# Optimization experiments

Measured on AMD Instinct MI355X. Metric: run time of the kernel, lower is better.

Reference implementation:

```python
import jax, jax.numpy as jnp
import numpy as np

DROPOUT_P = 0.5


def spmm(edge_weight, src, dst, x, n_nodes):
    # out[i] = sum_{e: dst[e]==i} edge_weight[e] * x[src[e]]  == spmm(adj, x)
    msgs = x[src] * edge_weight[:, None]          # [E, F]
    return jax.ops.segment_sum(msgs, dst, num_segments=n_nodes)


def setup_inputs() -> dict:
    key = jax.random.key(0)
    ks = jax.random.split(key, 7)
    N, E, F_IN, F_HID, F_OUT = 100000, 1600000, 128, 128, 64
    return {
        "x": jax.random.normal(ks[0], (N, F_IN), dtype=jnp.float32),
        "edge_weight": jax.random.uniform(ks[1], (E,), dtype=jnp.float32),
        "W1": jax.random.normal(ks[2], (F_IN, F_HID), dtype=jnp.float32) * 0.05,
        "b1": jnp.zeros((F_HID,), dtype=jnp.float32),
        "W2": jax.random.normal(ks[3], (F_HID, F_OUT), dtype=jnp.float32) * 0.05,
        "b2": jnp.zeros((F_OUT,), dtype=jnp.float32),
        "src": jax.random.randint(ks[4], (E,), 0, N, dtype=jnp.int32),
        "dst": jax.random.randint(ks[5], (E,), 0, N, dtype=jnp.int32),
        "n_nodes": N,
    }


def reference(x, edge_weight, W1, b1, W2, b2, src, dst, n_nodes):
    # layer 1: relu(Linear(spmm(adj, x)))
    h = spmm(edge_weight, src, dst, x, n_nodes)
    h = jax.nn.relu(h @ W1 + b1)
    # dropout (training=True), deterministic fixed key for reproducibility
    keep = jax.random.bernoulli(jax.random.key(42), 1.0 - DROPOUT_P, h.shape)
    h = jnp.where(keep, h / (1.0 - DROPOUT_P), 0.0)
    # layer 2: Linear(spmm(adj, h))
    h = spmm(edge_weight, src, dst, h, n_nodes)
    return h @ W2 + b2
```

## Files before the change

kernel.cpp:

```cpp
#include <hip/hip_runtime.h>

typedef unsigned int u32;
typedef unsigned short u16;
typedef __attribute__((ext_vector_type(8))) short short8;
typedef __attribute__((ext_vector_type(8))) unsigned short u16x8;
typedef __attribute__((ext_vector_type(4))) float f32x4;
typedef __attribute__((ext_vector_type(4))) unsigned short u16x4;

#define CAP 10240

__device__ __forceinline__ u16 f2bf(float f) {
  u32 u = __builtin_bit_cast(u32, f);
  u32 r = (u + 0x7fffu + ((u >> 16) & 1u)) >> 16;
  return (u16)r;
}
__device__ __forceinline__ float bf2f(u32 lo16) {
  return __builtin_bit_cast(float, lo16 << 16);
}

__device__ __forceinline__ void threefry2x32(u32 k0, u32 k1, u32 x0, u32 x1,
                                             u32& y0, u32& y1) {
  const u32 ks2 = k0 ^ k1 ^ 0x1BD11BDAu;
#define TFR(r) { x0 += x1; x1 = (x1 << (r)) | (x1 >> (32 - (r))); x1 ^= x0; }
  x0 += k0; x1 += k1;
  TFR(13) TFR(15) TFR(26) TFR(6)
  x0 += k1; x1 += ks2 + 1u;
  TFR(17) TFR(29) TFR(16) TFR(24)
  x0 += ks2; x1 += k0 + 2u;
  TFR(13) TFR(15) TFR(26) TFR(6)
  x0 += k0; x1 += k1 + 3u;
  TFR(17) TFR(29) TFR(16) TFR(24)
  x0 += k1; x1 += ks2 + 4u;
  TFR(13) TFR(15) TFR(26) TFR(6)
  x0 += ks2; x1 += k0 + 5u;
#undef TFR
  y0 = x0; y1 = x1;
}

__device__ __forceinline__ bool dropout_keep(u32 j) {
  u32 y0, y1;
  threefry2x32(0u, 42u, 0u, j, y0, y1);
  return ((y0 ^ y1) & 0x80000000u) == 0u;
}

__global__ __launch_bounds__(256) void init_bcur(int* __restrict__ bcur) {
  bcur[threadIdx.x] = threadIdx.x * CAP;
}

#define EPB 8192

__global__ __launch_bounds__(256) void stage_edges(
    const int* __restrict__ src, const int* __restrict__ dst,
    const float* __restrict__ ew, int* __restrict__ bcur,
    int2* __restrict__ staged, int E) {
  __shared__ int h[256];
  __shared__ int cb[256];
  int t = threadIdx.x;
  h[t] = 0;
  __syncthreads();
  int base = blockIdx.x * EPB;
  int end = min(base + EPB, E);
  for (int i = base + t; i < end; i += 256)
    atomicAdd(&h[(u32)dst[i] >> 9], 1);
  __syncthreads();
  if (h[t]) cb[t] = atomicAdd(&bcur[t], h[t]);
  h[t] = 0;
  __syncthreads();
  for (int i = base + t; i < end; i += 256) {
    int d = dst[i];
    int b = (u32)d >> 9;
    int loc = atomicAdd(&h[b], 1);
    int pos = cb[b] + loc;
    if (pos < (b + 1) * CAP)
      staged[pos] = make_int2(src[i] | ((d & 511) << 23),
                              __builtin_bit_cast(int, ew[i]));
  }
}

__global__ __launch_bounds__(256) void bucket_sort(
    const int2* __restrict__ staged, const int* __restrict__ bcur,
    int2* __restrict__ rowinfo, int2* __restrict__ epk, int N) {
  __shared__ int cnt[512];
  __shared__ int cur[512];
  __shared__ int sc[256];
  const int t = threadIdx.x;
  const int b = blockIdx.x;
  const int node0 = b << 9;
  const int nn = min(512, N - node0);
  const int ebase = b * CAP;
  const int ecnt = min(bcur[b] - ebase, CAP);
  cnt[t] = 0; cnt[t + 256] = 0;
  __syncthreads();
  for (int i = t; i < ecnt; i += 256)
    atomicAdd(&cnt[(u32)staged[ebase + i].x >> 23], 1);
  __syncthreads();
  int a = cnt[2 * t], c = cnt[2 * t + 1];
  int pa = (a + 1) & ~1, pc = (c + 1) & ~1;
  int s = pa + pc;
  sc[t] = s;
  __syncthreads();
  for (int off = 1; off < 256; off <<= 1) {
    int tmp = (t >= off) ? sc[t - off] : 0;
    __syncthreads();
    sc[t] += tmp;
    __syncthreads();
  }
  int excl = sc[t] - s;
  cur[2 * t] = ebase + excl;
  cur[2 * t + 1] = ebase + excl + pa;
  if (2 * t < nn) rowinfo[node0 + 2 * t] = make_int2(ebase + excl, a);
  if (2 * t + 1 < nn) rowinfo[node0 + 2 * t + 1] = make_int2(ebase + excl + pa, c);
  __syncthreads();
  for (int i = t; i < ecnt; i += 256) {
    int2 p = staged[ebase + i];
    int dl = (u32)p.x >> 23;
    int pos = atomicAdd(&cur[dl], 1);
    epk[pos] = make_int2(p.x & 0x7fffff, p.y);
  }
}

__global__ __launch_bounds__(256) void spmm_csr_f128_bf16(
    const u16* __restrict__ V, const int2* __restrict__ epk,
    const int2* __restrict__ rowinfo, u16* __restrict__ out, int N) {
  int node = blockIdx.x * 8 + (threadIdx.x >> 5);
  if (node >= N) return;
  int l32 = threadIdx.x & 31;
  int2 ri = rowinfo[node];
  int e = ri.x, end = ri.x + ri.y;
  float a0 = 0.f, a1 = 0.f, a2 = 0.f, a3 = 0.f;
  for (; e + 8 <= end; e += 8) {
    int4 pp[4];
#pragma unroll
    for (int k = 0; k < 4; ++k)
      pp[k] = reinterpret_cast<const int4*>(epk + e)[k];
    uint2 v[8];
#pragma unroll
    for (int k = 0; k < 4; ++k) {
      v[2 * k] = reinterpret_cast<const uint2*>(V + (size_t)pp[k].x * 128)[l32];
      v[2 * k + 1] = reinterpret_cast<const uint2*>(V + (size_t)pp[k].z * 128)[l32];
    }
#pragma unroll
    for (int k = 0; k < 4; ++k) {
      float w0 = __builtin_bit_cast(float, pp[k].y);
      float w1 = __builtin_bit_cast(float, pp[k].w);
      a0 = fmaf(bf2f(v[2 * k].x & 0xffffu), w0, a0);
      a1 = fmaf(bf2f(v[2 * k].x >> 16), w0, a1);
      a2 = fmaf(bf2f(v[2 * k].y & 0xffffu), w0, a2);
      a3 = fmaf(bf2f(v[2 * k].y >> 16), w0, a3);
      a0 = fmaf(bf2f(v[2 * k + 1].x & 0xffffu), w1, a0);
      a1 = fmaf(bf2f(v[2 * k + 1].x >> 16), w1, a1);
      a2 = fmaf(bf2f(v[2 * k + 1].y & 0xffffu), w1, a2);
      a3 = fmaf(bf2f(v[2 * k + 1].y >> 16), w1, a3);
    }
  }
  if (e + 4 <= end) {
    int4 pp[2];
#pragma unroll
    for (int k = 0; k < 2; ++k)
      pp[k] = reinterpret_cast<const int4*>(epk + e)[k];
    uint2 v[4];
#pragma unroll
    for (int k = 0; k < 2; ++k) {
      v[2 * k] = reinterpret_cast<const uint2*>(V + (size_t)pp[k].x * 128)[l32];
      v[2 * k + 1] = reinterpret_cast<const uint2*>(V + (size_t)pp[k].z * 128)[l32];
    }
#pragma unroll
    for (int k = 0; k < 2; ++k) {
      float w0 = __builtin_bit_cast(float, pp[k].y);
      float w1 = __builtin_bit_cast(float, pp[k].w);
      a0 = fmaf(bf2f(v[2 * k].x & 0xffffu), w0, a0);
      a1 = fmaf(bf2f(v[2 * k].x >> 16), w0, a1);
      a2 = fmaf(bf2f(v[2 * k].y & 0xffffu), w0, a2);
      a3 = fmaf(bf2f(v[2 * k].y >> 16), w0, a3);
      a0 = fmaf(bf2f(v[2 * k + 1].x & 0xffffu), w1, a0);
      a1 = fmaf(bf2f(v[2 * k + 1].x >> 16), w1, a1);
      a2 = fmaf(bf2f(v[2 * k + 1].y & 0xffffu), w1, a2);
      a3 = fmaf(bf2f(v[2 * k + 1].y >> 16), w1, a3);
    }
    e += 4;
  }
  for (; e < end; ++e) {
    int2 p = epk[e];
    uint2 v = reinterpret_cast<const uint2*>(V + (size_t)p.x * 128)[l32];
    float w = __builtin_bit_cast(float, p.y);
    a0 = fmaf(bf2f(v.x & 0xffffu), w, a0);
    a1 = fmaf(bf2f(v.x >> 16), w, a1);
    a2 = fmaf(bf2f(v.y & 0xffffu), w, a2);
    a3 = fmaf(bf2f(v.y >> 16), w, a3);
  }
  uint2 o;
  o.x = (u32)f2bf(a0) | ((u32)f2bf(a1) << 16);
  o.y = (u32)f2bf(a2) | ((u32)f2bf(a3) << 16);
  reinterpret_cast<uint2*>(out + (size_t)node * 128)[l32] = o;
}

__global__ __launch_bounds__(256) void spmm_csr_f64_bias(
    const u16* __restrict__ V, const int2* __restrict__ epk,
    const int2* __restrict__ rowinfo, const float* __restrict__ b2,
    float* __restrict__ out, int N) {
  int node = blockIdx.x * 16 + (threadIdx.x >> 4);
  if (node >= N) return;
  int l16 = threadIdx.x & 15;
  int2 ri = rowinfo[node];
  int e = ri.x, end = ri.x + ri.y;
  float4 bb = reinterpret_cast<const float4*>(b2)[l16];
  float a0 = bb.x, a1 = bb.y, a2 = bb.z, a3 = bb.w;
  for (; e + 8 <= end; e += 8) {
    int4 pp[4];
#pragma unroll
    for (int k = 0; k < 4; ++k)
      pp[k] = reinterpret_cast<const int4*>(epk + e)[k];
    uint2 v[8];
#pragma unroll
    for (int k = 0; k < 4; ++k) {
      v[2 * k] = reinterpret_cast<const uint2*>(V + (size_t)pp[k].x * 64)[l16];
      v[2 * k + 1] = reinterpret_cast<const uint2*>(V + (size_t)pp[k].z * 64)[l16];
    }
#pragma unroll
    for (int k = 0; k < 4; ++k) {
      float w0 = __builtin_bit_cast(float, pp[k].y);
      float w1 = __builtin_bit_cast(float, pp[k].w);
      a0 = fmaf(bf2f(v[2 * k].x & 0xffffu), w0, a0);
      a1 = fmaf(bf2f(v[2 * k].x >> 16), w0, a1);
      a2 = fmaf(bf2f(v[2 * k].y & 0xffffu), w0, a2);
      a3 = fmaf(bf2f(v[2 * k].y >> 16), w0, a3);
      a0 = fmaf(bf2f(v[2 * k + 1].x & 0xffffu), w1, a0);
      a1 = fmaf(bf2f(v[2 * k + 1].x >> 16), w1, a1);
      a2 = fmaf(bf2f(v[2 * k + 1].y & 0xffffu), w1, a2);
      a3 = fmaf(bf2f(v[2 * k + 1].y >> 16), w1, a3);
    }
  }
  for (; e < end; ++e) {
    int2 p = epk[e];
    uint2 v = reinterpret_cast<const uint2*>(V + (size_t)p.x * 64)[l16];
    float w = __builtin_bit_cast(float, p.y);
    a0 = fmaf(bf2f(v.x & 0xffffu), w, a0);
    a1 = fmaf(bf2f(v.x >> 16), w, a1);
    a2 = fmaf(bf2f(v.y & 0xffffu), w, a2);
    a3 = fmaf(bf2f(v.y >> 16), w, a3);
  }
  reinterpret_cast<float4*>(out + (size_t)node * 64)[l16] =
      make_float4(a0, a1, a2, a3);
}

__global__ __launch_bounds__(256) void gemm_xw1_mfma(
    const float* __restrict__ X, const float* __restrict__ W,
    u16* __restrict__ Y, int N) {
  __shared__ short As[128 * 128];
  __shared__ short Bs[128 * 128];
  const int t = threadIdx.x;
  const int row0 = blockIdx.x << 7;

  for (int i = t; i < 128 * 32; i += 256) {
    int m = i >> 5, k4 = i & 31;
    int r = row0 + m;
    float4 v = make_float4(0.f, 0.f, 0.f, 0.f);
    if (r < N) v = reinterpret_cast<const float4*>(X)[(size_t)r * 32 + k4];
    u16x4 b;
    b.x = f2bf(v.x); b.y = f2bf(v.y); b.z = f2bf(v.z); b.w = f2bf(v.w);
    int off = (m * 128 + (k4 << 2)) ^ ((m & 7) << 3);
    *reinterpret_cast<u16x4*>(&As[off]) = b;
  }
  for (int i = t; i < 128 * 32; i += 256) {
    int k = i >> 5, n4 = i & 31;
    float4 v = reinterpret_cast<const float4*>(W)[(size_t)k * 32 + n4];
    int c0 = n4 << 2;
    Bs[(((c0 + 0) * 128 + k)) ^ (((c0 + 0) & 7) << 3)] = (short)f2bf(v.x);
    Bs[(((c0 + 1) * 128 + k)) ^ (((c0 + 1) & 7) << 3)] = (short)f2bf(v.y);
    Bs[(((c0 + 2) * 128 + k)) ^ (((c0 + 2) & 7) << 3)] = (short)f2bf(v.z);
    Bs[(((c0 + 3) * 128 + k)) ^ (((c0 + 3) & 7) << 3)] = (short)f2bf(v.w);
  }
  __syncthreads();

  const int wid = t >> 6, lane = t & 63;
  const int wr = (wid >> 1) * 64, wc = (wid & 1) * 64;
  const int l15 = lane & 15, lk = (lane >> 4) * 8;

  f32x4 acc[4][4];
#pragma unroll
  for (int m = 0; m < 4; ++m)
#pragma unroll
    for (int n = 0; n < 4; ++n) acc[m][n] = (f32x4)(0.f);

#pragma unroll
  for (int kk = 0; kk < 4; ++kk) {
    const int kb = kk * 32 + lk;
    short8 a[4], b[4];
#pragma unroll
    for (int m = 0; m < 4; ++m) {
      int row = wr + m * 16 + l15;
      a[m] = *reinterpret_cast<const short8*>(&As[(row * 128 + kb) ^ ((row & 7) << 3)]);
    }
#pragma unroll
    for (int n = 0; n < 4; ++n) {
      int col = wc + n * 16 + l15;
      b[n] = *reinterpret_cast<const short8*>(&Bs[(col * 128 + kb) ^ ((col & 7) << 3)]);
    }
#pragma unroll
    for (int m = 0; m < 4; ++m)
#pragma unroll
      for (int n = 0; n < 4; ++n)
        acc[m][n] = __builtin_amdgcn_mfma_f32_16x16x32_bf16(a[m], b[n], acc[m][n], 0, 0, 0);
  }

#pragma unroll
  for (int m = 0; m < 4; ++m) {
    int rbase = row0 + wr + m * 16 + (lane >> 4) * 4;
#pragma unroll
    for (int n = 0; n < 4; ++n) {
      int col = wc + n * 16 + l15;
#pragma unroll
      for (int r = 0; r < 4; ++r) {
        int row = rbase + r;
        if (row < N) Y[(size_t)row * 128 + col] = f2bf(acc[m][n][r]);
      }
    }
  }
}

__global__ __launch_bounds__(256) void gemm_h_w2_mfma(
    const u16* __restrict__ H, const float* __restrict__ bias1,
    const float* __restrict__ W2, u16* __restrict__ O, int N) {
  __shared__ short As[128 * 128];
  __shared__ short Bs[64 * 128];
  const int t = threadIdx.x;
  const int row0 = blockIdx.x << 7;

  for (int i = t; i < 128 * 16; i += 256) {
    int k = i >> 4, n4 = i & 15;
    float4 v = reinterpret_cast<const float4*>(W2)[(size_t)k * 16 + n4];
    int c0 = n4 << 2;
    Bs[(((c0 + 0) * 128 + k)) ^ (((c0 + 0) & 7) << 3)] = (short)f2bf(v.x);
    Bs[(((c0 + 1) * 128 + k)) ^ (((c0 + 1) & 7) << 3)] = (short)f2bf(v.y);
    Bs[(((c0 + 2) * 128 + k)) ^ (((c0 + 2) & 7) << 3)] = (short)f2bf(v.z);
    Bs[(((c0 + 3) * 128 + k)) ^ (((c0 + 3) & 7) << 3)] = (short)f2bf(v.w);
  }

  for (int i = t; i < 128 * 16; i += 256) {
    int m = i >> 4, g = i & 15;
    int r = row0 + m;
    int c0 = g << 3;
    u16x8 o = (u16x8)(0);
    if (r < N) {
      u16x8 v = *reinterpret_cast<const u16x8*>(H + (size_t)r * 128 + c0);
      float4 b0 = reinterpret_cast<const float4*>(bias1)[g * 2];
      float4 b1v = reinterpret_cast<const float4*>(bias1)[g * 2 + 1];
      float bb[8] = {b0.x, b0.y, b0.z, b0.w, b1v.x, b1v.y, b1v.z, b1v.w};
      u32 base = (u32)r * 128u + (u32)c0;
#pragma unroll
      for (int e = 0; e < 8; ++e) {
        float z = fmaxf(bf2f((u16)v[e]) + bb[e], 0.f);
        o[e] = dropout_keep(base + e) ? f2bf(z + z) : (u16)0;
      }
    }
    *reinterpret_cast<u16x8*>(&As[(m * 128 + c0) ^ ((m & 7) << 3)]) = o;
  }
  __syncthreads();

  const int wid = t >> 6, lane = t & 63;
  const int wr = wid * 32;
  const int l15 = lane & 15, lk = (lane >> 4) * 8;

  f32x4 acc[2][4];
#pragma unroll
  for (int m = 0; m < 2; ++m)
#pragma unroll
    for (int n = 0; n < 4; ++n) acc[m][n] = (f32x4)(0.f);

#pragma unroll
  for (int kk = 0; kk < 4; ++kk) {
    const int kb = kk * 32 + lk;
    short8 a[2], b[4];
#pragma unroll
    for (int m = 0; m < 2; ++m) {
      int row = wr + m * 16 + l15;
      a[m] = *reinterpret_cast<const short8*>(&As[(row * 128 + kb) ^ ((row & 7) << 3)]);
    }
#pragma unroll
    for (int n = 0; n < 4; ++n) {
      int col = n * 16 + l15;
      b[n] = *reinterpret_cast<const short8*>(&Bs[(col * 128 + kb) ^ ((col & 7) << 3)]);
    }
#pragma unroll
    for (int m = 0; m < 2; ++m)
#pragma unroll
      for (int n = 0; n < 4; ++n)
        acc[m][n] = __builtin_amdgcn_mfma_f32_16x16x32_bf16(a[m], b[n], acc[m][n], 0, 0, 0);
  }

#pragma unroll
  for (int m = 0; m < 2; ++m) {
    int rbase = row0 + wr + m * 16 + (lane >> 4) * 4;
#pragma unroll
    for (int n = 0; n < 4; ++n) {
      int col = n * 16 + l15;
#pragma unroll
      for (int r = 0; r < 4; ++r) {
        int row = rbase + r;
        if (row < N) O[(size_t)row * 64 + col] = f2bf(acc[m][n][r]);
      }
    }
  }
}

extern "C" void kernel_launch(void* const* d_in, const int* in_sizes, int n_in,
                              void* d_out, int out_size, void* d_ws, size_t ws_size,
                              hipStream_t stream) {
  const float* x  = (const float*)d_in[0];
  const float* ew = (const float*)d_in[1];
  const float* W1 = (const float*)d_in[2];
  const float* b1 = (const float*)d_in[3];
  const float* W2 = (const float*)d_in[4];
  const float* b2 = (const float*)d_in[5];
  const int*   src = (const int*)d_in[6];
  const int*   dst = (const int*)d_in[7];
  const int N = in_sizes[0] / 128;
  const int E = in_sizes[1];
  float* out = (float*)d_out;

  const int nb = (N + 511) >> 9;

  u16*   h1      = (u16*)d_ws;
  u16*   y       = h1 + (size_t)N * 128;
  u16*   h3      = y;
  int2*  staged  = (int2*)(y + (size_t)N * 128);
  int2*  epk     = staged + (size_t)nb * CAP;
  int2*  rowinfo = epk + (size_t)nb * CAP;
  int*   bcur    = (int*)(rowinfo + N + 4);

  const int cBlocks = (E + EPB - 1) / EPB;
  const int gBlocks = (N + 127) / 128;

  init_bcur<<<1, 256, 0, stream>>>(bcur);
  stage_edges<<<cBlocks, 256, 0, stream>>>(src, dst, ew, bcur, staged, E);
  bucket_sort<<<nb, 256, 0, stream>>>(staged, bcur, rowinfo, epk, N);

  gemm_xw1_mfma<<<gBlocks, 256, 0, stream>>>(x, W1, y, N);
  spmm_csr_f128_bf16<<<(N + 7) / 8, 256, 0, stream>>>(y, epk, rowinfo, h1, N);
  gemm_h_w2_mfma<<<gBlocks, 256, 0, stream>>>(h1, b1, W2, h3, N);
  spmm_csr_f64_bias<<<(N + 15) / 16, 256, 0, stream>>>(h3, epk, rowinfo, b2, out, N);
}
```

Measured before the change: 245.9 us.

## Fuse edge staging into X·W1 GEMM launch and shrink buckets to 256 nodes

After: 234.8 us. 1.05x faster.

```diff
diff --git a/kernel.cpp b/kernel.cpp
--- a/kernel.cpp
+++ b/kernel.cpp
@@ -7,7 +7,8 @@
 typedef __attribute__((ext_vector_type(4))) float f32x4;
 typedef __attribute__((ext_vector_type(4))) unsigned short u16x4;
 
-#define CAP 10240
+#define CAP 4864
+#define EPB 8192
 
 __device__ __forceinline__ u16 f2bf(float f) {
   u32 u = __builtin_bit_cast(u32, f);
@@ -43,61 +44,132 @@
   return ((y0 ^ y1) & 0x80000000u) == 0u;
 }
 
-__global__ __launch_bounds__(256) void init_bcur(int* __restrict__ bcur) {
-  bcur[threadIdx.x] = threadIdx.x * CAP;
-}
-
-#define EPB 8192
-
-__global__ __launch_bounds__(256) void stage_edges(
+__global__ __launch_bounds__(256) void gemmA_stage_fused(
+    const float* __restrict__ X, const float* __restrict__ W,
+    u16* __restrict__ Y, int N, int cBlocks,
     const int* __restrict__ src, const int* __restrict__ dst,
     const float* __restrict__ ew, int* __restrict__ bcur,
-    int2* __restrict__ staged, int E) {
-  __shared__ int h[256];
-  __shared__ int cb[256];
-  int t = threadIdx.x;
-  h[t] = 0;
-  __syncthreads();
-  int base = blockIdx.x * EPB;
-  int end = min(base + EPB, E);
-  for (int i = base + t; i < end; i += 256)
-    atomicAdd(&h[(u32)dst[i] >> 9], 1);
-  __syncthreads();
-  if (h[t]) cb[t] = atomicAdd(&bcur[t], h[t]);
-  h[t] = 0;
-  __syncthreads();
-  for (int i = base + t; i < end; i += 256) {
-    int d = dst[i];
-    int b = (u32)d >> 9;
-    int loc = atomicAdd(&h[b], 1);
-    int pos = cb[b] + loc;
-    if (pos < (b + 1) * CAP)
-      staged[pos] = make_int2(src[i] | ((d & 511) << 23),
-                              __builtin_bit_cast(int, ew[i]));
+    int2* __restrict__ staged, int E, int nb) {
+  __shared__ short As[128 * 128];
+  __shared__ short Bs[128 * 128];
+  const int t = threadIdx.x;
+
+  if (blockIdx.x < cBlocks) {
+    int* h  = (int*)As;
+    int* cb = ((int*)As) + 512;
+    for (int j = t; j < nb; j += 256) h[j] = 0;
+    __syncthreads();
+    const int base = blockIdx.x * EPB;
+    const int end = min(base + EPB, E);
+    for (int i = base + t; i < end; i += 256)
+      atomicAdd(&h[(u32)dst[i] >> 8], 1);
+    __syncthreads();
+    for (int j = t; j < nb; j += 256) {
+      cb[j] = h[j] ? atomicAdd(&bcur[j], h[j]) : 0;
+      h[j] = 0;
+    }
+    __syncthreads();
+    for (int i = base + t; i < end; i += 256) {
+      int d = dst[i];
+      int b = (u32)d >> 8;
+      int loc = atomicAdd(&h[b], 1);
+      int pos = cb[b] + loc;
+      if (pos < CAP)
+        staged[(size_t)b * CAP + pos] =
+            make_int2(src[i] | ((d & 255) << 23), __builtin_bit_cast(int, ew[i]));
+    }
+    return;
+  }
+
+  const int row0 = (blockIdx.x - cBlocks) << 7;
+
+  for (int i = t; i < 128 * 32; i += 256) {
+    int m = i >> 5, k4 = i & 31;
+    int r = row0 + m;
+    float4 v = make_float4(0.f, 0.f, 0.f, 0.f);
+    if (r < N) v = reinterpret_cast<const float4*>(X)[(size_t)r * 32 + k4];
+    u16x4 b;
+    b.x = f2bf(v.x); b.y = f2bf(v.y); b.z = f2bf(v.z); b.w = f2bf(v.w);
+    int off = (m * 128 + (k4 << 2)) ^ ((m & 7) << 3);
+    *reinterpret_cast<u16x4*>(&As[off]) = b;
+  }
+  for (int i = t; i < 128 * 32; i += 256) {
+    int k = i >> 5, n4 = i & 31;
+    float4 v = reinterpret_cast<const float4*>(W)[(size_t)k * 32 + n4];
+    int c0 = n4 << 2;
+    Bs[(((c0 + 0) * 128 + k)) ^ (((c0 + 0) & 7) << 3)] = (short)f2bf(v.x);
+    Bs[(((c0 + 1) * 128 + k)) ^ (((c0 + 1) & 7) << 3)] = (short)f2bf(v.y);
+    Bs[(((c0 + 2) * 128 + k)) ^ (((c0 + 2) & 7) << 3)] = (short)f2bf(v.z);
+    Bs[(((c0 + 3) * 128 + k)) ^ (((c0 + 3) & 7) << 3)] = (short)f2bf(v.w);
+  }
+  __syncthreads();
+
+  const int wid = t >> 6, lane = t & 63;
+  const int wr = (wid >> 1) * 64, wc = (wid & 1) * 64;
+  const int l15 = lane & 15, lk = (lane >> 4) * 8;
+
+  f32x4 acc[4][4];
+#pragma unroll
+  for (int m = 0; m < 4; ++m)
+#pragma unroll
+    for (int n = 0; n < 4; ++n) acc[m][n] = (f32x4)(0.f);
+
+#pragma unroll
+  for (int kk = 0; kk < 4; ++kk) {
+    const int kb = kk * 32 + lk;
+    short8 a[4], b[4];
+#pragma unroll
+    for (int m = 0; m < 4; ++m) {
+      int row = wr + m * 16 + l15;
+      a[m] = *reinterpret_cast<const short8*>(&As[(row * 128 + kb) ^ ((row & 7) << 3)]);
+    }
+#pragma unroll
+    for (int n = 0; n < 4; ++n) {
+      int col = wc + n * 16 + l15;
+      b[n] = *reinterpret_cast<const short8*>(&Bs[(col * 128 + kb) ^ ((col & 7) << 3)]);
+    }
+#pragma unroll
+    for (int m = 0; m < 4; ++m)
+#pragma unroll
+      for (int n = 0; n < 4; ++n)
+        acc[m][n] = __builtin_amdgcn_mfma_f32_16x16x32_bf16(a[m], b[n], acc[m][n], 0, 0, 0);
+  }
+
+#pragma unroll
+  for (int m = 0; m < 4; ++m) {
+    int rbase = row0 + wr + m * 16 + (lane >> 4) * 4;
+#pragma unroll
+    for (int n = 0; n < 4; ++n) {
+      int col = wc + n * 16 + l15;
+#pragma unroll
+      for (int r = 0; r < 4; ++r) {
+        int row = rbase + r;
+        if (row < N) Y[(size_t)row * 128 + col] = f2bf(acc[m][n][r]);
+      }
+    }
   }
 }
 
 __global__ __launch_bounds__(256) void bucket_sort(
     const int2* __restrict__ staged, const int* __restrict__ bcur,
     int2* __restrict__ rowinfo, int2* __restrict__ epk, int N) {
-  __shared__ int cnt[512];
-  __shared__ int cur[512];
+  __shared__ int cnt[256];
+  __shared__ int cur[256];
   __shared__ int sc[256];
   const int t = threadIdx.x;
   const int b = blockIdx.x;
-  const int node0 = b << 9;
-  const int nn = min(512, N - node0);
+  const int node0 = b << 8;
+  const int nn = min(256, N - node0);
   const int ebase = b * CAP;
-  const int ecnt = min(bcur[b] - ebase, CAP);
-  cnt[t] = 0; cnt[t + 256] = 0;
+  const int ecnt = min(bcur[b], CAP);
+  cnt[t] = 0;
   __syncthreads();
   for (int i = t; i < ecnt; i += 256)
     atomicAdd(&cnt[(u32)staged[ebase + i].x >> 23], 1);
   __syncthreads();
-  int a = cnt[2 * t], c = cnt[2 * t + 1];
-  int pa = (a + 1) & ~1, pc = (c + 1) & ~1;
-  int s = pa + pc;
-  sc[t] = s;
+  int a = cnt[t];
+  int pa = (a + 1) & ~1;
+  sc[t] = pa;
   __syncthreads();
   for (int off = 1; off < 256; off <<= 1) {
     int tmp = (t >= off) ? sc[t - off] : 0;
@@ -105,11 +177,9 @@
     sc[t] += tmp;
     __syncthreads();
   }
-  int excl = sc[t] - s;
-  cur[2 * t] = ebase + excl;
-  cur[2 * t + 1] = ebase + excl + pa;
-  if (2 * t < nn) rowinfo[node0 + 2 * t] = make_int2(ebase + excl, a);
-  if (2 * t + 1 < nn) rowinfo[node0 + 2 * t + 1] = make_int2(ebase + excl + pa, c);
+  int excl = sc[t] - pa;
+  cur[t] = ebase + excl;
+  if (t < nn) rowinfo[node0 + t] = make_int2(ebase + excl, a);
   __syncthreads();
   for (int i = t; i < ecnt; i += 256) {
     int2 p = staged[ebase + i];
@@ -118,6 +188,18 @@
     epk[pos] = make_int2(p.x & 0x7fffff, p.y);
   }
 }
+
+#define F128_FMA2(VA, VB, W0, W1)                      \
+  { float w0 = __builtin_bit_cast(float, W0);          \
+    float w1 = __builtin_bit_cast(float, W1);          \
+    a0 = fmaf(bf2f((VA).x & 0xffffu), w0, a0);         \
+    a1 = fmaf(bf2f((VA).x >> 16), w0, a1);             \
+    a2 = fmaf(bf2f((VA).y & 0xffffu), w0, a2);         \
+    a3 = fmaf(bf2f((VA).y >> 16), w0, a3);             \
+    a0 = fmaf(bf2f((VB).x & 0xffffu), w1, a0);         \
+    a1 = fmaf(bf2f((VB).x >> 16), w1, a1);             \
+    a2 = fmaf(bf2f((VB).y & 0xffffu), w1, a2);         \
+    a3 = fmaf(bf2f((VB).y >> 16), w1, a3); }
 
 __global__ __launch_bounds__(256) void spmm_csr_f128_bf16(
     const u16* __restrict__ V, const int2* __restrict__ epk,
@@ -128,32 +210,22 @@
   int2 ri = rowinfo[node];
   int e = ri.x, end = ri.x + ri.y;
   float a0 = 0.f, a1 = 0.f, a2 = 0.f, a3 = 0.f;
-  for (; e + 8 <= end; e += 8) {
-    int4 pp[4];
-#pragma unroll
-    for (int k = 0; k < 4; ++k)
+  for (; e + 16 <= end; e += 16) {
+    int4 pp[8];
+#pragma unroll
+    for (int k = 0; k < 8; ++k)
       pp[k] = reinterpret_cast<const int4*>(epk + e)[k];
-    uint2 v[8];
-#pragma unroll
-    for (int k = 0; k < 4; ++k) {
+    uint2 v[16];
+#pragma unroll
+    for (int k = 0; k < 8; ++k) {
       v[2 * k] = reinterpret_cast<const uint2*>(V + (size_t)pp[k].x * 128)[l32];
       v[2 * k + 1] = reinterpret_cast<const uint2*>(V + (size_t)pp[k].z * 128)[l32];
     }
 #pragma unroll
-    for (int k = 0; k < 4; ++k) {
-      float w0 = __builtin_bit_cast(float, pp[k].y);
-      float w1 = __builtin_bit_cast(float, pp[k].w);
-      a0 = fmaf(bf2f(v[2 * k].x & 0xffffu), w0, a0);
-      a1 = fmaf(bf2f(v[2 * k].x >> 16), w0, a1);
-      a2 = fmaf(bf2f(v[2 * k].y & 0xffffu), w0, a2);
-      a3 = fmaf(bf2f(v[2 * k].y >> 16), w0, a3);
-      a0 = fmaf(bf2f(v[2 * k + 1].x & 0xffffu), w1, a0);
-      a1 = fmaf(bf2f(v[2 * k + 1].x >> 16), w1, a1);
-      a2 = fmaf(bf2f(v[2 * k + 1].y & 0xffffu), w1, a2);
-      a3 = fmaf(bf2f(v[2 * k + 1].y >> 16), w1, a3);
-    }
-  }
-  if (e + 4 <= end) {
+    for (int k = 0; k < 8; ++k)
+      F128_FMA2(v[2 * k], v[2 * k + 1], pp[k].y, pp[k].w);
+  }
+  for (; e + 4 <= end; e += 4) {
     int4 pp[2];
 #pragma unroll
     for (int k = 0; k < 2; ++k)
@@ -165,19 +237,8 @@
       v[2 * k + 1] = reinterpret_cast<const uint2*>(V + (size_t)pp[k].z * 128)[l32];
     }
 #pragma unroll
-    for (int k = 0; k < 2; ++k) {
-      float w0 = __builtin_bit_cast(float, pp[k].y);
-      float w1 = __builtin_bit_cast(float, pp[k].w);
-      a0 = fmaf(bf2f(v[2 * k].x & 0xffffu), w0, a0);
-      a1 = fmaf(bf2f(v[2 * k].x >> 16), w0, a1);
-      a2 = fmaf(bf2f(v[2 * k].y & 0xffffu), w0, a2);
-      a3 = fmaf(bf2f(v[2 * k].y >> 16), w0, a3);
-      a0 = fmaf(bf2f(v[2 * k + 1].x & 0xffffu), w1, a0);
-      a1 = fmaf(bf2f(v[2 * k + 1].x >> 16), w1, a1);
-      a2 = fmaf(bf2f(v[2 * k + 1].y & 0xffffu), w1, a2);
-      a3 = fmaf(bf2f(v[2 * k + 1].y >> 16), w1, a3);
-    }
-    e += 4;
+    for (int k = 0; k < 2; ++k)
+      F128_FMA2(v[2 * k], v[2 * k + 1], pp[k].y, pp[k].w);
   }
   for (; e < end; ++e) {
     int2 p = epk[e];
@@ -205,30 +266,35 @@
   int e = ri.x, end = ri.x + ri.y;
   float4 bb = reinterpret_cast<const float4*>(b2)[l16];
   float a0 = bb.x, a1 = bb.y, a2 = bb.z, a3 = bb.w;
-  for (; e + 8 <= end; e += 8) {
-    int4 pp[4];
-#pragma unroll
-    for (int k = 0; k < 4; ++k)
+  for (; e + 16 <= end; e += 16) {
+    int4 pp[8];
+#pragma unroll
+    for (int k = 0; k < 8; ++k)
       pp[k] = reinterpret_cast<const int4*>(epk + e)[k];
-    uint2 v[8];
-#pragma unroll
-    for (int k = 0; k < 4; ++k) {
+    uint2 v[16];
+#pragma unroll
+    for (int k = 0; k < 8; ++k) {
       v[2 * k] = reinterpret_cast<const uint2*>(V + (size_t)pp[k].x * 64)[l16];
       v[2 * k + 1] = reinterpret_cast<const uint2*>(V + (size_t)pp[k].z * 64)[l16];
     }
 #pragma unroll
-    for (int k = 0; k < 4; ++k) {
-      float w0 = __builtin_bit_cast(float, pp[k].y);
-      float w1 = __builtin_bit_cast(float, pp[k].w);
-      a0 = fmaf(bf2f(v[2 * k].x & 0xffffu), w0, a0);
-      a1 = fmaf(bf2f(v[2 * k].x >> 16), w0, a1);
-      a2 = fmaf(bf2f(v[2 * k].y & 0xffffu), w0, a2);
-      a3 = fmaf(bf2f(v[2 * k].y >> 16), w0, a3);
-      a0 = fmaf(bf2f(v[2 * k + 1].x & 0xffffu), w1, a0);
-      a1 = fmaf(bf2f(v[2 * k + 1].x >> 16), w1, a1);
-      a2 = fmaf(bf2f(v[2 * k + 1].y & 0xffffu), w1, a2);
-      a3 = fmaf(bf2f(v[2 * k + 1].y >> 16), w1, a3);
-    }
+    for (int k = 0; k < 8; ++k)
+      F128_FMA2(v[2 * k], v[2 * k + 1], pp[k].y, pp[k].w);
+  }
+  for (; e + 4 <= end; e += 4) {
+    int4 pp[2];
+#pragma unroll
+    for (int k = 0; k < 2; ++k)
+      pp[k] = reinterpret_cast<const int4*>(epk + e)[k];
+    uint2 v[4];
+#pragma unroll
+    for (int k = 0; k < 2; ++k) {
+      v[2 * k] = reinterpret_cast<const uint2*>(V + (size_t)pp[k].x * 64)[l16];
+      v[2 * k + 1] = reinterpret_cast<const uint2*>(V + (size_t)pp[k].z * 64)[l16];
+    }
+#pragma unroll
+    for (int k = 0; k < 2; ++k)
+      F128_FMA2(v[2 * k], v[2 * k + 1], pp[k].y, pp[k].w);
   }
   for (; e < end; ++e) {
     int2 p = epk[e];
@@ -241,81 +307,6 @@
   }
   reinterpret_cast<float4*>(out + (size_t)node * 64)[l16] =
       make_float4(a0, a1, a2, a3);
-}
-
-__global__ __launch_bounds__(256) void gemm_xw1_mfma(
-    const float* __restrict__ X, const float* __restrict__ W,
-    u16* __restrict__ Y, int N) {
-  __shared__ short As[128 * 128];
-  __shared__ short Bs[128 * 128];
-  const int t = threadIdx.x;
-  const int row0 = blockIdx.x << 7;
-
-  for (int i = t; i < 128 * 32; i += 256) {
-    int m = i >> 5, k4 = i & 31;
-    int r = row0 + m;
-    float4 v = make_float4(0.f, 0.f, 0.f, 0.f);
-    if (r < N) v = reinterpret_cast<const float4*>(X)[(size_t)r * 32 + k4];
-    u16x4 b;
-    b.x = f2bf(v.x); b.y = f2bf(v.y); b.z = f2bf(v.z); b.w = f2bf(v.w);
-    int off = (m * 128 + (k4 << 2)) ^ ((m & 7) << 3);
-    *reinterpret_cast<u16x4*>(&As[off]) = b;
-  }
-  for (int i = t; i < 128 * 32; i += 256) {
-    int k = i >> 5, n4 = i & 31;
-    float4 v = reinterpret_cast<const float4*>(W)[(size_t)k * 32 + n4];
-    int c0 = n4 << 2;
-    Bs[(((c0 + 0) * 128 + k)) ^ (((c0 + 0) & 7) << 3)] = (short)f2bf(v.x);
-    Bs[(((c0 + 1) * 128 + k)) ^ (((c0 + 1) & 7) << 3)] = (short)f2bf(v.y);
-    Bs[(((c0 + 2) * 128 + k)) ^ (((c0 + 2) & 7) << 3)] = (short)f2bf(v.z);
-    Bs[(((c0 + 3) * 128 + k)) ^ (((c0 + 3) & 7) << 3)] = (short)f2bf(v.w);
-  }
-  __syncthreads();
-
-  const int wid = t >> 6, lane = t & 63;
-  const int wr = (wid >> 1) * 64, wc = (wid & 1) * 64;
-  const int l15 = lane & 15, lk = (lane >> 4) * 8;
-
-  f32x4 acc[4][4];
-#pragma unroll
-  for (int m = 0; m < 4; ++m)
-#pragma unroll
-    for (int n = 0; n < 4; ++n) acc[m][n] = (f32x4)(0.f);
-
-#pragma unroll
-  for (int kk = 0; kk < 4; ++kk) {
-    const int kb = kk * 32 + lk;
-    short8 a[4], b[4];
-#pragma unroll
-    for (int m = 0; m < 4; ++m) {
-      int row = wr + m * 16 + l15;
-      a[m] = *reinterpret_cast<const short8*>(&As[(row * 128 + kb) ^ ((row & 7) << 3)]);
-    }
-#pragma unroll
-    for (int n = 0; n < 4; ++n) {
-      int col = wc + n * 16 + l15;
-      b[n] = *reinterpret_cast<const short8*>(&Bs[(col * 128 + kb) ^ ((col & 7) << 3)]);
-    }
-#pragma unroll
-    for (int m = 0; m < 4; ++m)
-#pragma unroll
-      for (int n = 0; n < 4; ++n)
-        acc[m][n] = __builtin_amdgcn_mfma_f32_16x16x32_bf16(a[m], b[n], acc[m][n], 0, 0, 0);
-  }
-
-#pragma unroll
-  for (int m = 0; m < 4; ++m) {
-    int rbase = row0 + wr + m * 16 + (lane >> 4) * 4;
-#pragma unroll
-    for (int n = 0; n < 4; ++n) {
-      int col = wc + n * 16 + l15;
-#pragma unroll
-      for (int r = 0; r < 4; ++r) {
-        int row = rbase + r;
-        if (row < N) Y[(size_t)row * 128 + col] = f2bf(acc[m][n][r]);
-      }
-    }
-  }
 }
 
 __global__ __launch_bounds__(256) void gemm_h_w2_mfma(
@@ -418,7 +409,7 @@
   const int E = in_sizes[1];
   float* out = (float*)d_out;
 
-  const int nb = (N + 511) >> 9;
+  const int nb = (N + 255) >> 8;
 
   u16*   h1      = (u16*)d_ws;
   u16*   y       = h1 + (size_t)N * 128;
@@ -431,11 +422,10 @@
   const int cBlocks = (E + EPB - 1) / EPB;
   const int gBlocks = (N + 127) / 128;
 
-  init_bcur<<<1, 256, 0, stream>>>(bcur);
-  stage_edges<<<cBlocks, 256, 0, stream>>>(src, dst, ew, bcur, staged, E);
+  hipMemsetAsync(bcur, 0, (size_t)nb * sizeof(int), stream);
+  gemmA_stage_fused<<<cBlocks + gBlocks, 256, 0, stream>>>(
+      x, W1, y, N, cBlocks, src, dst, ew, bcur, staged, E, nb);
   bucket_sort<<<nb, 256, 0, stream>>>(staged, bcur, rowinfo, epk, N);
-
-  gemm_xw1_mfma<<<gBlocks, 256, 0, stream>>>(x, W1, y, N);
   spmm_csr_f128_bf16<<<(N + 7) / 8, 256, 0, stream>>>(y, epk, rowinfo, h1, N);
   gemm_h_w2_mfma<<<gBlocks, 256, 0, stream>>>(h1, b1, W2, h3, N);
   spmm_csr_f64_bias<<<(N + 15) / 16, 256, 0, stream>>>(h3, epk, rowinfo, b2, out, N);
```
